# Kernel optimization log

Hardware: AMD Instinct MI355X
Metric: run time of the kernel (lower is better)

## Reference

```python
import jax, jax.numpy as jnp
import numpy as np

# skimage color deconvolution constants: hed_from_rgb = inv(rgb_from_hed)
_RGB_FROM_HED = np.array([[0.65, 0.70, 0.29],
                          [0.07, 0.99, 0.11],
                          [0.27, 0.57, 0.78]], dtype=np.float64)
_HED_FROM_RGB = np.linalg.inv(_RGB_FROM_HED).astype(np.float32)
_LOG_ADJUST = float(np.log(1e-6))  # skimage separate_stains log base


def setup_inputs() -> dict:
    key = jax.random.key(0)
    k1, = jax.random.split(key, 1)
    x = jax.random.uniform(k1, (64, 3, 512, 512), dtype=jnp.float32)  # RGB patches in [0,1]
    gamma = jnp.ones((1,), dtype=jnp.float32)   # InstanceNorm2d affine weight
    beta = jnp.zeros((1,), dtype=jnp.float32)   # InstanceNorm2d affine bias
    return {"x": x, "gamma": gamma, "beta": beta}


def reference(x, gamma, beta):
    h_weights = jnp.asarray(_HED_FROM_RGB[:, 0])  # only H (hematoxylin) column needed, shape (3,)

    # --- skimage.color.separate_stains, batched (replaces per-sample CPU loop) ---
    rgb = jnp.clip(x, 0.0, 1.0)                  # torch.clamp(t, 0, 1)
    rgb = jnp.maximum(rgb, 1e-6)                 # avoid log(0)
    od = jnp.log(rgb) / _LOG_ADJUST              # optical density, (B,3,H,W)
    h = jnp.einsum('bchw,c->bhw', od, h_weights) # stain matrix multiply, H channel only
    h = jnp.maximum(h, 0.0)[:, None, :, :]       # (B,1,H,W), skimage clips stains at 0

    # --- FFT magnitude spectrum ---
    fft = jnp.fft.fft2(h, norm='forward')        # complex64, scaled by 1/(H*W)
    fft = jnp.fft.fftshift(fft, axes=(-2, -1))
    mag = jnp.abs(fft)

    # --- _normalize_log_fft: log1p then per-image min-max ---
    log_mag = jnp.log1p(mag)
    mn = jnp.min(log_mag, axis=(-2, -1), keepdims=True)
    mx = jnp.max(log_mag, axis=(-2, -1), keepdims=True)
    rng = mx - mn
    safe_rng = jnp.where(rng > 0, rng, 1.0)
    normed = jnp.where(rng > 0, (log_mag - mn) / safe_rng, 0.0)

    # --- nn.InstanceNorm2d(1, affine=True), eps=1e-5 ---
    mu = jnp.mean(normed, axis=(-2, -1), keepdims=True)
    var = jnp.var(normed, axis=(-2, -1), keepdims=True)
    out = (normed - mu) * jax.lax.rsqrt(var + 1e-5)
    return out * gamma[None, :, None, None] + beta[None, :, None, None]
```

## Files before the change

### kernel.cpp

```cpp
#include <hip/hip_runtime.h>
#include <hip/hip_fp16.h>
#include <math.h>


#define PI_F 3.14159265358979323846f
#define FROW 264
#define LMSTR 264
#define LVMAX 1.6f
#define QE (65535.0f / LVMAX)
#define QD (LVMAX / 65535.0f)
#define XSTR 568

__device__ __forceinline__ int MU(int p) {
    return ((p >> 6) * 72) + (p & 56) + ((p & 7) ^ ((p >> 3) & 7));
}
__device__ __forceinline__ int odrev(int k) {
    return ((k & 7) << 6) | (k & 56) | (k >> 6);
}

__device__ __forceinline__ float2 cadd(float2 a, float2 b) { return make_float2(a.x + b.x, a.y + b.y); }
__device__ __forceinline__ float2 csub(float2 a, float2 b) { return make_float2(a.x - b.x, a.y - b.y); }
__device__ __forceinline__ float2 cmul(float2 a, float2 w) {
    return make_float2(a.x * w.x - a.y * w.y, a.x * w.y + a.y * w.x);
}

__device__ __forceinline__ void dft8(float2 v[8]) {
    const float s = 0.70710678118654752f;
    float2 a0 = cadd(v[0], v[4]), b0 = csub(v[0], v[4]);
    float2 a1 = cadd(v[1], v[5]), b1 = csub(v[1], v[5]);
    float2 a2 = cadd(v[2], v[6]), b2 = csub(v[2], v[6]);
    float2 a3 = cadd(v[3], v[7]), b3 = csub(v[3], v[7]);
    b1 = make_float2(s * (b1.x + b1.y), s * (b1.y - b1.x));
    b2 = make_float2(b2.y, -b2.x);
    b3 = make_float2(s * (b3.y - b3.x), -s * (b3.x + b3.y));
    float2 c0 = cadd(a0, a2), c1 = cadd(a1, a3);
    float2 d0 = csub(a0, a2), d1 = csub(a1, a3);
    d1 = make_float2(d1.y, -d1.x);
    v[0] = cadd(c0, c1); v[4] = csub(c0, c1);
    v[2] = cadd(d0, d1); v[6] = csub(d0, d1);
    float2 e0 = cadd(b0, b2), e1 = cadd(b1, b3);
    float2 f0 = csub(b0, b2), f1 = csub(b1, b3);
    f1 = make_float2(f1.y, -f1.x);
    v[1] = cadd(e0, e1); v[5] = csub(e0, e1);
    v[3] = cadd(f0, f1); v[7] = csub(f0, f1);
}

__device__ __forceinline__ void fft512_reg(float2* Xw, const float2* TW, int lane) {
    float2 v[8];
    #pragma unroll
    for (int m = 0; m < 8; ++m) v[m] = Xw[MU(lane + (m << 6))];
    dft8(v);
    #pragma unroll
    for (int m = 1; m < 8; ++m) v[m] = cmul(v[m], TW[(lane * m) & 511]);
    #pragma unroll
    for (int m = 0; m < 8; ++m) Xw[MU((m << 6) + lane)] = v[m];
    __builtin_amdgcn_wave_barrier();
    const int b = lane >> 3, t = lane & 7;
    const int base2 = (b << 6) + t;
    #pragma unroll
    for (int m = 0; m < 8; ++m) v[m] = Xw[MU(base2 + (m << 3))];
    dft8(v);
    #pragma unroll
    for (int m = 1; m < 8; ++m) v[m] = cmul(v[m], TW[(t * m) << 3]);
    #pragma unroll
    for (int m = 0; m < 8; ++m) Xw[MU(base2 + (m << 3))] = v[m];
    __builtin_amdgcn_wave_barrier();
    const int base3 = (b << 6) + (t << 3);
    #pragma unroll
    for (int j = 0; j < 8; ++j) v[j] = Xw[MU(base3 + j)];
    dft8(v);
    #pragma unroll
    for (int sidx = 0; sidx < 8; ++sidx) Xw[MU(base3 + sidx)] = v[sidx];
    __builtin_amdgcn_wave_barrier();
}

__device__ __forceinline__ void hstore(float2* Xw, int c,
                                       float r0v, float g0v, float b0v,
                                       float r1v, float g1v, float b1v,
                                       float w0, float w1, float w2) {
    r0v = fminf(fmaxf(r0v, 1e-6f), 1.0f);
    g0v = fminf(fmaxf(g0v, 1e-6f), 1.0f);
    b0v = fminf(fmaxf(b0v, 1e-6f), 1.0f);
    r1v = fminf(fmaxf(r1v, 1e-6f), 1.0f);
    g1v = fminf(fmaxf(g1v, 1e-6f), 1.0f);
    b1v = fminf(fmaxf(b1v, 1e-6f), 1.0f);
    float h0 = fmaxf(w0 * __log2f(r0v) + w1 * __log2f(g0v) + w2 * __log2f(b0v), 0.0f);
    float h1 = fmaxf(w0 * __log2f(r1v) + w1 * __log2f(g1v) + w2 * __log2f(b1v), 0.0f);
    Xw[MU(c)] = make_float2(h0, h1);
}

__global__ __launch_bounds__(256) void k_rowfft(const float* __restrict__ x,
                                                __half2* __restrict__ Fh,
                                                float w0, float w1, float w2) {
    const int b = blockIdx.x >> 6;
    const int p = blockIdx.x & 63;
    __shared__ float2 X[4 * XSTR];
    __shared__ float2 TW[512];
    const int tid = threadIdx.x;
    const int w = tid >> 6, lane = tid & 63;
    #pragma unroll
    for (int t = 0; t < 8; ++t) {
        int idx = lane + (t << 6);
        float sn, cs;
        __sincosf(-PI_F * (float)idx * (1.0f / 256.0f), &sn, &cs);
        TW[idx] = make_float2(cs, sn);
    }
    float2* Xw = X + w * XSTR;
    const float* xb = x + (size_t)b * 786432;
    const int r0 = (p << 3) + (w << 1);

    #pragma unroll
    for (int q = 0; q < 2; ++q) {
        const int cb = (q << 8) + (lane << 2);
        float4 R0 = *(const float4*)(xb +          (r0 << 9) + cb);
        float4 G0 = *(const float4*)(xb + 262144 + (r0 << 9) + cb);
        float4 B0 = *(const float4*)(xb + 524288 + (r0 << 9) + cb);
        float4 R1 = *(const float4*)(xb +          ((r0 + 1) << 9) + cb);
        float4 G1 = *(const float4*)(xb + 262144 + ((r0 + 1) << 9) + cb);
        float4 B1 = *(const float4*)(xb + 524288 + ((r0 + 1) << 9) + cb);
        hstore(Xw, cb + 0, R0.x, G0.x, B0.x, R1.x, G1.x, B1.x, w0, w1, w2);
        hstore(Xw, cb + 1, R0.y, G0.y, B0.y, R1.y, G1.y, B1.y, w0, w1, w2);
        hstore(Xw, cb + 2, R0.z, G0.z, B0.z, R1.z, G1.z, B1.z, w0, w1, w2);
        hstore(Xw, cb + 3, R0.w, G0.w, B0.w, R1.w, G1.w, B1.w, w0, w1, w2);
    }
    __builtin_amdgcn_wave_barrier();

    fft512_reg(Xw, TW, lane);

    __half2* Fb = Fh + (size_t)b * (512 * FROW);
    #pragma unroll
    for (int t = 0; t < 4; ++t) {
        int k = lane + (t << 6);
        int m = (512 - k) & 511;
        float2 zk = Xw[MU(odrev(k))];
        float2 zm = Xw[MU(odrev(m))];
        Fb[r0 * FROW + k]       = __floats2half2_rn(0.5f * (zk.x + zm.x),  0.5f * (zk.y - zm.y));
        Fb[(r0 + 1) * FROW + k] = __floats2half2_rn(0.5f * (zk.y + zm.y), -0.5f * (zk.x - zm.x));
    }
    if (lane == 0) {
        float2 z = Xw[MU(odrev(256))];
        Fb[r0 * FROW + 256]       = __floats2half2_rn(z.x, 0.0f);
        Fb[(r0 + 1) * FROW + 256] = __floats2half2_rn(z.y, 0.0f);
    }
}

__global__ __launch_bounds__(512) void k_colfft(const __half2* __restrict__ Fh,
                                                unsigned short* __restrict__ lmu,
                                                float4* __restrict__ partials) {
    const int b = blockIdx.x >> 4;
    const int g = blockIdx.x & 15;
    __shared__ float2 X[8 * XSTR];
    __shared__ float2 TW[512];
    __shared__ float4 wred[8];
    const int tid = threadIdx.x;
    const int w = tid >> 6, lane = tid & 63;
    {
        float sn, cs;
        __sincosf(-PI_F * (float)tid * (1.0f / 256.0f), &sn, &cs);
        TW[tid] = make_float2(cs, sn);
    }
    const __half2* Fb = Fh + (size_t)b * (512 * FROW);
    unsigned short* lm_b = lmu + (size_t)b * (512 * LMSTR);
    float mn = 1e30f, mx = -1e30f, s1 = 0.0f, s2 = 0.0f;

    for (int pass = 0; pass < 2; ++pass) {
        const int u0 = (g << 4) + (pass << 3);
        const bool packpass = (g == 0 && pass == 0);
        __syncthreads();
        for (int i = tid; i < 4096; i += 512) {
            int y = i >> 3, c = i & 7;
            float2 v;
            if (packpass && c == 0) {
                float2 f0   = __half22float2(Fb[y * FROW]);
                float2 f256 = __half22float2(Fb[y * FROW + 256]);
                v = make_float2(f0.x, f256.x);
            } else {
                v = __half22float2(Fb[y * FROW + u0 + c]);
            }
            X[c * XSTR + MU(y)] = v;
        }
        __syncthreads();
        fft512_reg(X + w * XSTR, TW, lane);
        __syncthreads();
        for (int i = tid; i < 4096; i += 512) {
            int k = i >> 3, c = i & 7;
            int ro = (k + 256) & 511;
            if (packpass && c == 0) {
                int m = (512 - k) & 511;
                float2 zk = X[MU(odrev(k))];
                float2 zm = X[MU(odrev(m))];
                float2 c0   = make_float2(0.5f * (zk.x + zm.x),  0.5f * (zk.y - zm.y));
                float2 c256 = make_float2(0.5f * (zk.y + zm.y), -0.5f * (zk.x - zm.x));
                float lv0   = __log2f(1.0f + sqrtf(c0.x * c0.x + c0.y * c0.y));
                float lv256 = __log2f(1.0f + sqrtf(c256.x * c256.x + c256.y * c256.y));
                unsigned q0 = (unsigned)__float2uint_rn(fminf(lv0,   LVMAX) * QE);
                unsigned q6 = (unsigned)__float2uint_rn(fminf(lv256, LVMAX) * QE);
                lm_b[ro * LMSTR]       = (unsigned short)q0;
                lm_b[ro * LMSTR + 256] = (unsigned short)q6;
                mn = fminf(mn, fminf(lv0, lv256));
                mx = fmaxf(mx, fmaxf(lv0, lv256));
                s1 += lv0 + lv256;
                s2 += lv0 * lv0 + lv256 * lv256;
            } else {
                int u = u0 + c;
                float2 v = X[c * XSTR + MU(odrev(k))];
                float lv = __log2f(1.0f + sqrtf(v.x * v.x + v.y * v.y));
                unsigned q = (unsigned)__float2uint_rn(fminf(lv, LVMAX) * QE);
                lm_b[ro * LMSTR + u] = (unsigned short)q;
                mn = fminf(mn, lv);
                mx = fmaxf(mx, lv);
                s1 += 2.0f * lv;
                s2 += 2.0f * lv * lv;
            }
        }
    }

    #pragma unroll
    for (int off = 32; off > 0; off >>= 1) {
        mn = fminf(mn, __shfl_down(mn, off, 64));
        mx = fmaxf(mx, __shfl_down(mx, off, 64));
        s1 += __shfl_down(s1, off, 64);
        s2 += __shfl_down(s2, off, 64);
    }
    if (lane == 0) wred[w] = make_float4(mn, mx, s1, s2);
    __syncthreads();
    if (tid == 0) {
        float4 r = wred[0];
        #pragma unroll
        for (int wv = 1; wv < 8; ++wv) {
            float4 q2 = wred[wv];
            r.x = fminf(r.x, q2.x);
            r.y = fmaxf(r.y, q2.y);
            r.z += q2.z;
            r.w += q2.w;
        }
        partials[blockIdx.x] = r;
    }
}

__global__ __launch_bounds__(64) void k_coeff(const float4* __restrict__ partials,
                                              const float* __restrict__ gamma,
                                              const float* __restrict__ beta,
                                              float2* __restrict__ coeff) {
    const int b = blockIdx.x;
    float mn = 1e30f, mx = -1e30f, s1 = 0.0f, s2 = 0.0f;
    if (threadIdx.x < 16) {
        float4 r = partials[(b << 4) + threadIdx.x];
        mn = r.x; mx = r.y; s1 = r.z; s2 = r.w;
    }
    #pragma unroll
    for (int off = 32; off > 0; off >>= 1) {
        mn = fminf(mn, __shfl_down(mn, off, 64));
        mx = fmaxf(mx, __shfl_down(mx, off, 64));
        s1 += __shfl_down(s1, off, 64);
        s2 += __shfl_down(s2, off, 64);
    }
    if (threadIdx.x == 0) {
        const float N = 262144.0f;
        float mean = s1 / N;
        float var = fmaxf(s2 / N - mean * mean, 0.0f);
        float rng = mx - mn;
        float g = gamma[0], bt = beta[0];
        float A, B;
        if (rng > 0.0f) {
            float inv = 1.0f / rng;
            float varn = var * inv * inv;
            float sc = 1.0f / sqrtf(varn + 1e-5f);
            A = g * sc * inv;
            B = bt - mean * A;
        } else {
            A = 0.0f;
            B = bt;
        }
        coeff[b] = make_float2(A, B);
    }
}

__global__ __launch_bounds__(256) void k_norm(const unsigned short* __restrict__ lmu,
                                              float* __restrict__ out,
                                              const float2* __restrict__ coeff) {
    const int j = blockIdx.x & 63;
    const int b = blockIdx.x >> 6;
    __shared__ unsigned short L[8][260];
    const float2 ab = coeff[b];
    const float A = ab.x, B = ab.y;
    const unsigned short* lb = lmu + (size_t)b * (512 * LMSTR);
    float* ob = out + ((size_t)b << 18);
    const int tid = threadIdx.x;

    auto rowOf = [&](int row8) -> int {
        int q = row8 >> 1, h = row8 & 1;
        int p = (j << 2) + q;
        return h ? ((p == 0) ? 256 : 512 - p) : p;
    };

    for (int i = tid; i < 8 * 65; i += 256) {
        int row8 = i / 65, c4 = i % 65;
        int r = rowOf(row8);
        const unsigned short* Ld = lb + (size_t)r * LMSTR;
        if (c4 < 64) {
            *(uint2*)&L[row8][c4 << 2] = *(const uint2*)&Ld[c4 << 2];
        } else {
            L[row8][256] = Ld[256];
        }
    }
    __syncthreads();

    for (int i = tid; i < 1024; i += 256) {
        int row8 = i >> 7, f4 = i & 127;
        int co = f4 << 2;
        int r = rowOf(row8);
        int p = (j << 2) + (row8 >> 1);
        int m8 = (p == 0) ? row8 : (row8 ^ 1);
        float4 o;
        if (f4 >= 64) {
            int u = co - 256;
            o.x = (float)L[row8][u]     * QD * A + B;
            o.y = (float)L[row8][u + 1] * QD * A + B;
            o.z = (float)L[row8][u + 2] * QD * A + B;
            o.w = (float)L[row8][u + 3] * QD * A + B;
        } else {
            o.x = ((co == 0) ? (float)L[row8][256]
                             : (float)L[m8][256 - co]) * QD * A + B;
            o.y = (float)L[m8][255 - co] * QD * A + B;
            o.z = (float)L[m8][254 - co] * QD * A + B;
            o.w = (float)L[m8][253 - co] * QD * A + B;
        }
        *(float4*)&ob[(r << 9) + co] = o;
    }
}

extern "C" void kernel_launch(void* const* d_in, const int* in_sizes, int n_in,
                              void* d_out, int out_size, void* d_ws, size_t ws_size,
                              hipStream_t stream) {
    const float* x     = (const float*)d_in[0];
    const float* gamma = (const float*)d_in[1];
    const float* beta  = (const float*)d_in[2];
    float* out = (float*)d_out;

    __half2* Fh = (__half2*)d_ws;
    unsigned short* lmu = (unsigned short*)((char*)d_ws + ((size_t)40 << 20));
    float4* partials = (float4*)((char*)d_ws + ((size_t)60 << 20));
    float2* coeff    = (float2*)((char*)d_ws + ((size_t)60 << 20) + 16384);

    const double M00=0.65, M01=0.70, M02=0.29;
    const double M10=0.07, M11=0.99, M12=0.11;
    const double M20=0.27, M21=0.57, M22=0.78;
    const double det = M00*(M11*M22 - M12*M21)
                     - M01*(M10*M22 - M12*M20)
                     + M02*(M10*M21 - M11*M20);
    const float hw0 = (float)( (M11*M22 - M12*M21) / det);
    const float hw1 = (float)(-(M10*M22 - M12*M20) / det);
    const float hw2 = (float)( (M10*M21 - M11*M20) / det);
    const float invLA2 = (float)(log(2.0) / log(1e-6));
    const float sN = 1.0f / (512.0f * 512.0f);
    const float w0 = hw0 * invLA2 * sN;
    const float w1 = hw1 * invLA2 * sN;
    const float w2 = hw2 * invLA2 * sN;

    k_rowfft<<<64 * 64, 256, 0, stream>>>(x, Fh, w0, w1, w2);
    k_colfft<<<64 * 16, 512, 0, stream>>>(Fh, lmu, partials);
    k_coeff<<<64, 64, 0, stream>>>(partials, gamma, beta, coeff);
    k_norm<<<64 * 64, 256, 0, stream>>>(lmu, out, coeff);
}
```

Before: 115.7 us.

## Fuse column-FFT epilogue into registers and stage quantized output through LDS

The column FFT's last radix-8 pass now keeps its results in registers and computes the log-magnitude quantization directly, instead of writing back to LDS and re-reading in a separate loop. Quantized values go into a small LDS staging buffer and are then written to global memory as 8-byte vector stores per row, replacing scattered 2-byte stores. The packed-real wave keeps the old write-back path. This adds an extra LDS buffer and barrier but removes one LDS round trip and improves global store coalescing.

```diff
diff --git a/kernel.cpp b/kernel.cpp
--- a/kernel.cpp
+++ b/kernel.cpp
@@ -10,6 +10,7 @@
 #define QE (65535.0f / LVMAX)
 #define QD (LVMAX / 65535.0f)
 #define XSTR 568
+#define RS 12
 
 __device__ __forceinline__ int MU(int p) {
     return ((p >> 6) * 72) + (p & 56) + ((p & 7) ^ ((p >> 3) & 7));
@@ -45,7 +46,7 @@
     v[3] = cadd(f0, f1); v[7] = csub(f0, f1);
 }
 
-__device__ __forceinline__ void fft512_reg(float2* Xw, const float2* TW, int lane) {
+__device__ __forceinline__ void fft512_p12(float2* Xw, const float2* TW, int lane) {
     float2 v[8];
     #pragma unroll
     for (int m = 0; m < 8; ++m) v[m] = Xw[MU(lane + (m << 6))];
@@ -65,10 +66,22 @@
     #pragma unroll
     for (int m = 0; m < 8; ++m) Xw[MU(base2 + (m << 3))] = v[m];
     __builtin_amdgcn_wave_barrier();
+}
+
+__device__ __forceinline__ void fft512_p3(float2* Xw, int lane, float2 v[8]) {
+    const int b = lane >> 3, t = lane & 7;
     const int base3 = (b << 6) + (t << 3);
     #pragma unroll
     for (int j = 0; j < 8; ++j) v[j] = Xw[MU(base3 + j)];
     dft8(v);
+}
+
+__device__ __forceinline__ void fft512_reg(float2* Xw, const float2* TW, int lane) {
+    fft512_p12(Xw, TW, lane);
+    float2 v[8];
+    fft512_p3(Xw, lane, v);
+    const int b = lane >> 3, t = lane & 7;
+    const int base3 = (b << 6) + (t << 3);
     #pragma unroll
     for (int sidx = 0; sidx < 8; ++sidx) Xw[MU(base3 + sidx)] = v[sidx];
     __builtin_amdgcn_wave_barrier();
@@ -151,6 +164,7 @@
     const int g = blockIdx.x & 15;
     __shared__ float2 X[8 * XSTR];
     __shared__ float2 TW[512];
+    __shared__ unsigned short stage[512 * RS];
     __shared__ float4 wred[8];
     const int tid = threadIdx.x;
     const int w = tid >> 6, lane = tid & 63;
@@ -180,38 +194,61 @@
             X[c * XSTR + MU(y)] = v;
         }
         __syncthreads();
-        fft512_reg(X + w * XSTR, TW, lane);
-        __syncthreads();
-        for (int i = tid; i < 4096; i += 512) {
-            int k = i >> 3, c = i & 7;
-            int ro = (k + 256) & 511;
-            if (packpass && c == 0) {
+        float2* Xc = X + w * XSTR;
+        fft512_p12(Xc, TW, lane);
+        float2 v[8];
+        fft512_p3(Xc, lane, v);
+        if (!(packpass && w == 0)) {
+            const int bb = lane >> 3, t = lane & 7;
+            #pragma unroll
+            for (int j = 0; j < 8; ++j) {
+                int k = (j << 6) + (t << 3) + bb;
+                float lv = __log2f(1.0f + sqrtf(v[j].x * v[j].x + v[j].y * v[j].y));
+                unsigned q = (unsigned)__float2uint_rn(fminf(lv, LVMAX) * QE);
+                stage[k * RS + w] = (unsigned short)q;
+                mn = fminf(mn, lv);
+                mx = fmaxf(mx, lv);
+                s1 += 2.0f * lv;
+                s2 += 2.0f * lv * lv;
+            }
+        } else {
+            const int bb = lane >> 3, t = lane & 7;
+            const int base3 = (bb << 6) + (t << 3);
+            #pragma unroll
+            for (int sidx = 0; sidx < 8; ++sidx) Xc[MU(base3 + sidx)] = v[sidx];
+            __builtin_amdgcn_wave_barrier();
+            #pragma unroll
+            for (int t2 = 0; t2 < 8; ++t2) {
+                int k = lane + (t2 << 6);
                 int m = (512 - k) & 511;
-                float2 zk = X[MU(odrev(k))];
-                float2 zm = X[MU(odrev(m))];
+                float2 zk = Xc[MU(odrev(k))];
+                float2 zm = Xc[MU(odrev(m))];
                 float2 c0   = make_float2(0.5f * (zk.x + zm.x),  0.5f * (zk.y - zm.y));
                 float2 c256 = make_float2(0.5f * (zk.y + zm.y), -0.5f * (zk.x - zm.x));
                 float lv0   = __log2f(1.0f + sqrtf(c0.x * c0.x + c0.y * c0.y));
                 float lv256 = __log2f(1.0f + sqrtf(c256.x * c256.x + c256.y * c256.y));
                 unsigned q0 = (unsigned)__float2uint_rn(fminf(lv0,   LVMAX) * QE);
                 unsigned q6 = (unsigned)__float2uint_rn(fminf(lv256, LVMAX) * QE);
-                lm_b[ro * LMSTR]       = (unsigned short)q0;
-                lm_b[ro * LMSTR + 256] = (unsigned short)q6;
+                stage[k * RS + 0] = (unsigned short)q0;
+                stage[k * RS + 8] = (unsigned short)q6;
                 mn = fminf(mn, fminf(lv0, lv256));
                 mx = fmaxf(mx, fmaxf(lv0, lv256));
                 s1 += lv0 + lv256;
                 s2 += lv0 * lv0 + lv256 * lv256;
-            } else {
-                int u = u0 + c;
-                float2 v = X[c * XSTR + MU(odrev(k))];
-                float lv = __log2f(1.0f + sqrtf(v.x * v.x + v.y * v.y));
-                unsigned q = (unsigned)__float2uint_rn(fminf(lv, LVMAX) * QE);
-                lm_b[ro * LMSTR + u] = (unsigned short)q;
-                mn = fminf(mn, lv);
-                mx = fmaxf(mx, lv);
-                s1 += 2.0f * lv;
-                s2 += 2.0f * lv * lv;
             }
+        }
+        __syncthreads();
+        #pragma unroll
+        for (int it = 0; it < 2; ++it) {
+            int i2 = tid + (it << 9);
+            int ro = i2 >> 1, h = i2 & 1;
+            int k = ro ^ 256;
+            uint2 d = *(const uint2*)&stage[k * RS + (h << 2)];
+            *(uint2*)&lm_b[ro * LMSTR + u0 + (h << 2)] = d;
+        }
+        if (packpass) {
+            int ro = tid;
+            lm_b[ro * LMSTR + 256] = stage[(ro ^ 256) * RS + 8];
         }
     }
 
```

New measurement: 109.6 us. 1.06x faster.
